# Optimization experiments

Measured on AMD Instinct MI355X. Metric: run time of the kernel, lower is better.

## Reference

```python
import jax, jax.numpy as jnp
import numpy as np


def setup_inputs() -> dict:
    key = jax.random.key(0)
    k1, k2 = jax.random.split(key)
    B, C, H, L = 4, 1, 1024, 4096
    x = jax.random.normal(k1, (B, H, L), dtype=jnp.float32)
    k = jax.random.normal(k2, (C, H, L), dtype=jnp.float32)
    return {"x": x, "k": k}


def reference(x, k):
    # x: (B, H, L) input; k: (C, H, l_kernel) SSM convolution kernel.
    # FFT convolution with zero-padding to n = l_kernel + L (linear conv),
    # then truncate to the first L outputs (causal conv output).
    L = x.shape[-1]
    l_kernel = k.shape[-1]
    n = l_kernel + L
    k_f = jnp.fft.rfft(k, n=n)                       # (C, H, n//2+1) complex
    x_f = jnp.fft.rfft(x, n=n)                       # (B, H, n//2+1) complex
    y_f = jnp.einsum('bhl,chl->bchl', x_f, k_f)      # broadcast complex multiply
    y = jnp.fft.irfft(y_f, n=n)[..., :L]             # (B, C, H, L)
    return y
```

## Files before the change

### kernel.cpp

```cpp
#include <hip/hip_runtime.h>

#define THREADS 256
#define B_DIM   4
#define H_DIM   1024
#define L_DIM   4096
#define NFFT    4096
#define PI_F     3.14159265358979323846f
#define TWO_PI_F 6.28318530717958647692f

__device__ __forceinline__ float2 cmulf(float2 a, float2 b) {
    return make_float2(a.x*b.x - a.y*b.y, a.x*b.y + a.y*b.x);
}
__device__ __forceinline__ float2 caddf(float2 a, float2 b){ return make_float2(a.x+b.x, a.y+b.y); }
__device__ __forceinline__ float2 csubf(float2 a, float2 b){ return make_float2(a.x-b.x, a.y-b.y); }

__device__ __forceinline__ int swz(int i) { return i ^ ((i>>4)&15) ^ ((i>>8)&15); }

__device__ __forceinline__ void make_tw(float base, float2 w[16]) {
    float sn, cs; __sincosf(base, &sn, &cs);
    w[1]  = make_float2(cs, sn);
    w[2]  = cmulf(w[1], w[1]);
    w[3]  = cmulf(w[2], w[1]);
    w[4]  = cmulf(w[2], w[2]);
    w[5]  = cmulf(w[4], w[1]);
    w[6]  = cmulf(w[4], w[2]);
    w[7]  = cmulf(w[4], w[3]);
    w[8]  = cmulf(w[4], w[4]);
    w[9]  = cmulf(w[8], w[1]);
    w[10] = cmulf(w[8], w[2]);
    w[11] = cmulf(w[8], w[3]);
    w[12] = cmulf(w[8], w[4]);
    w[13] = cmulf(w[8], w[5]);
    w[14] = cmulf(w[8], w[6]);
    w[15] = cmulf(w[8], w[7]);
}

__device__ __forceinline__ float2 w16c(int q, float s) {
    constexpr float C[8] = {1.f, 0.9238795325f, 0.7071067812f, 0.3826834324f,
                            0.f, -0.3826834324f, -0.7071067812f, -0.9238795325f};
    constexpr float S[8] = {0.f, 0.3826834324f, 0.7071067812f, 0.9238795325f,
                            1.f, 0.9238795325f, 0.7071067812f, 0.3826834324f};
    return make_float2(C[q], s*S[q]);
}

template<int SGN>
__device__ __forceinline__ float2 twq(float2 d, int q) {
    if (q == 0) return d;
    if (q == 4) return make_float2((float)(-SGN)*d.y, (float)SGN*d.x);
    return cmulf(d, w16c(q, (float)SGN));
}

template<int SGN, bool HZ>
__device__ __forceinline__ void dif16(float2 v[16]) {
    if (HZ) {
        #pragma unroll
        for (int i = 0; i < 8; ++i) {
            float2 a = v[i];
            v[i+8] = twq<SGN>(a, i);
        }
    } else {
        #pragma unroll
        for (int i = 0; i < 8; ++i) {
            float2 a = v[i], b = v[i+8];
            v[i]   = caddf(a,b);
            v[i+8] = twq<SGN>(csubf(a,b), i);
        }
    }
    #pragma unroll
    for (int h = 4; h >= 1; h >>= 1) {
        const int step = 8 / h;
        #pragma unroll
        for (int g = 0; g < 16; g += 2*h) {
            #pragma unroll
            for (int i = 0; i < h; ++i) {
                float2 a = v[g+i], b = v[g+i+h];
                v[g+i]   = caddf(a,b);
                v[g+i+h] = twq<SGN>(csubf(a,b), i*step);
            }
        }
    }
}

template<int SGN>
__device__ __forceinline__ void dit16(float2 v[16]) {
    #pragma unroll
    for (int h = 1; h <= 8; h <<= 1) {
        const int step = 8 / h;
        #pragma unroll
        for (int g = 0; g < 16; g += 2*h) {
            #pragma unroll
            for (int i = 0; i < h; ++i) {
                float2 a = v[g+i];
                float2 b = twq<SGN>(v[g+i+h], i*step);
                v[g+i]   = caddf(a,b);
                v[g+i+h] = csubf(a,b);
            }
        }
    }
}

__device__ __constant__ int REV4_C[16] = {0,8,4,12,2,10,6,14,1,9,5,13,3,11,7,15};

__device__ __forceinline__ void fwd_fft_row(const float2* __restrict__ src, float2* Z, int t) {
    constexpr int REV4[16] = {0,8,4,12,2,10,6,14,1,9,5,13,3,11,7,15};
    float2 v[16], w[16];
    #pragma unroll
    for (int r = 0; r < 8; ++r) v[r] = src[256*r + t];
    dif16<-1, true>(v);
    make_tw(-TWO_PI_F * (float)t / (float)NFFT, w);
    #pragma unroll
    for (int kk = 1; kk < 16; ++kk) v[REV4[kk]] = cmulf(v[REV4[kk]], w[kk]);
    #pragma unroll
    for (int kk = 0; kk < 16; ++kk) Z[swz(256*kk + t)] = v[REV4[kk]];
    __syncthreads();

    const int k1 = t >> 4, m = t & 15;
    const int rb = 256*k1 + m;
    #pragma unroll
    for (int r = 0; r < 16; ++r) v[r] = Z[swz(rb + 16*r)];
    dif16<-1,false>(v);
    make_tw(-TWO_PI_F * (float)m / 256.f, w);
    #pragma unroll
    for (int kk = 1; kk < 16; ++kk) v[REV4[kk]] = cmulf(v[REV4[kk]], w[kk]);
    #pragma unroll
    for (int kk = 0; kk < 16; ++kk) Z[swz(rb + 16*kk)] = v[REV4[kk]];
    __syncthreads();

    const int b3 = t << 4;
    #pragma unroll
    for (int r = 0; r < 16; ++r) v[r] = Z[swz(b3 + r)];
    dif16<-1,false>(v);
    #pragma unroll
    for (int kk = 0; kk < 16; ++kk) Z[swz(b3 + kk)] = v[REV4[kk]];
}

__device__ __forceinline__ int binpos(int j) {
    return swz( ((j&15)<<8) | (((j>>4)&15)<<4) | (j>>8) );
}

__global__ __launch_bounds__(THREADS, 4)
void kfft_kernel(const float* __restrict__ k, float2* __restrict__ Kf_all) {
    __shared__ float2 Zk[NFFT];
    const int t  = threadIdx.x;
    const int hh = blockIdx.x;
    const float2* kp = (const float2*)(k + (size_t)hh * L_DIM);

    fwd_fft_row(kp, Zk, t);
    __syncthreads();

    float2* Kf = Kf_all + (size_t)hh * NFFT;
    #pragma unroll
    for (int s = 0; s < 8; ++s) {
        int j = t + 256*s;
        if (j == 0) {
            float2 zk = Zk[0];
            Kf[0] = make_float2(zk.x + zk.y, zk.x - zk.y);
            float2 zk2 = Zk[swz(8)];
            Kf[2048] = make_float2(zk2.x, -zk2.y);
        } else {
            int jm = NFFT - j;
            float2 zkj = Zk[binpos(j)], zkm = Zk[binpos(jm)];
            float sn, cs; __sincosf(-PI_F * (float)j / (float)NFFT, &sn, &cs);
            float2 w = make_float2(cs, sn);
            float2 Ke = make_float2(0.5f*(zkj.x + zkm.x), 0.5f*(zkj.y - zkm.y));
            float2 dk = make_float2(zkj.x - zkm.x, zkj.y + zkm.y);
            float2 Ko = make_float2(0.5f*dk.y, -0.5f*dk.x);
            float2 tk = cmulf(w, Ko);
            Kf[j]  = caddf(Ke, tk);
            Kf[jm] = make_float2(Ke.x - tk.x, -(Ke.y - tk.y));
        }
    }
}

__global__ __launch_bounds__(THREADS, 4)
void conv_main_kernel(const float* __restrict__ x, const float2* __restrict__ Kf_all,
                      float* __restrict__ out) {
    __shared__ float2 Zx[NFFT];
    constexpr int REV4[16] = {0,8,4,12,2,10,6,14,1,9,5,13,3,11,7,15};

    const int t  = threadIdx.x;
    const int wg = blockIdx.x;
    const int hh = wg & (H_DIM - 1);
    const int b  = wg >> 10;

    const float2* xp = (const float2*)(x + ((size_t)(b*H_DIM + hh)) * L_DIM);
    const float2* Kf = Kf_all + (size_t)hh * NFFT;

    fwd_fft_row(xp, Zx, t);

    float2 kfj[8], kfm[8], kf2;
    #pragma unroll
    for (int s = 0; s < 8; ++s) {
        int j = t + 256*s;
        kfj[s] = Kf[j];
        kfm[s] = Kf[(NFFT - j) & (NFFT - 1)];
    }
    kf2 = Kf[2048];
    __syncthreads();

    #pragma unroll
    for (int s = 0; s < 8; ++s) {
        int j = t + 256*s;
        if (j == 0) {
            float2 zx = Zx[0];
            float ax0 = zx.x + zx.y, axM = zx.x - zx.y;
            float y0 = ax0 * kfj[0].x, yM = axM * kfj[0].y;
            Zx[0] = make_float2(0.5f*(y0 + yM), 0.5f*(y0 - yM));
            int p2 = swz(8);
            float2 zx2 = Zx[p2];
            Zx[p2] = cmulf(zx2, make_float2(kf2.x, -kf2.y));
        } else {
            int jm = NFFT - j;
            int pj = binpos(j), pm = binpos(jm);
            float2 zxj = Zx[pj], zxm = Zx[pm];

            float sn, cs; __sincosf(-PI_F * (float)j / (float)NFFT, &sn, &cs);
            float2 w = make_float2(cs, sn);

            float2 Xe = make_float2(0.5f*(zxj.x + zxm.x), 0.5f*(zxj.y - zxm.y));
            float2 dx = make_float2(zxj.x - zxm.x, zxj.y + zxm.y);
            float2 Xo = make_float2(0.5f*dx.y, -0.5f*dx.x);
            float2 tx = cmulf(w, Xo);
            float2 Axj = caddf(Xe, tx);
            float2 Axm = make_float2(Xe.x - tx.x, -(Xe.y - tx.y));

            float2 Yj = cmulf(Axj, kfj[s]);
            float2 Ym = cmulf(Axm, kfm[s]);

            float2 u  = make_float2(0.5f*(Yj.x + Ym.x), 0.5f*(Yj.y - Ym.y));
            float2 dd = make_float2(Yj.x - Ym.x, Yj.y + Ym.y);
            float2 wc = make_float2(w.x, -w.y);
            float2 vv = cmulf(wc, dd);
            vv.x *= 0.5f; vv.y *= 0.5f;
            Zx[pj] = make_float2(u.x - vv.y, u.y + vv.x);
            Zx[pm] = make_float2(u.x + vv.y, -(u.y - vv.x));
        }
    }
    __syncthreads();

    float2 vx[16], w[16];
    const int k1 = t >> 4, m = t & 15;
    const int rb = 256*k1 + m;
    const int b3 = t << 4;

    #pragma unroll
    for (int r = 0; r < 16; ++r) vx[REV4[r]] = Zx[swz(b3 + r)];
    dit16<1>(vx);
    #pragma unroll
    for (int mm = 0; mm < 16; ++mm) Zx[swz(b3 + mm)] = vx[mm];
    __syncthreads();

    make_tw(TWO_PI_F * (float)m / 256.f, w);
    #pragma unroll
    for (int kk = 0; kk < 16; ++kk) {
        float2 val = Zx[swz(rb + 16*kk)];
        if (kk > 0) val = cmulf(val, w[kk]);
        vx[REV4[kk]] = val;
    }
    dit16<1>(vx);
    #pragma unroll
    for (int r = 0; r < 16; ++r) Zx[swz(rb + 16*r)] = vx[r];
    __syncthreads();

    make_tw(TWO_PI_F * (float)t / (float)NFFT, w);
    #pragma unroll
    for (int kk = 0; kk < 16; ++kk) {
        float2 val = Zx[swz(256*kk + t)];
        if (kk > 0) val = cmulf(val, w[kk]);
        vx[REV4[kk]] = val;
    }
    dit16<1>(vx);
    float2* op = (float2*)(out + ((size_t)(b*H_DIM + hh)) * L_DIM);
    const float sc = 1.f / (float)NFFT;
    #pragma unroll
    for (int n1 = 0; n1 < 8; ++n1) {
        float2 z = vx[n1];
        op[256*n1 + t] = make_float2(z.x*sc, z.y*sc);
    }
}

__global__ __launch_bounds__(THREADS, 2)
void fftconv_fallback(const float* __restrict__ x, const float* __restrict__ k,
                      float* __restrict__ out) {
    __shared__ float2 Zx[NFFT];
    __shared__ float2 Zk[NFFT];
    constexpr int REV4[16] = {0,8,4,12,2,10,6,14,1,9,5,13,3,11,7,15};

    const int t  = threadIdx.x;
    const int wg = blockIdx.x;
    const int hh = wg & (H_DIM - 1);
    const int b  = wg >> 10;

    const float2* xp = (const float2*)(x + ((size_t)(b*H_DIM + hh)) * L_DIM);
    const float2* kp = (const float2*)(k + (size_t)hh * L_DIM);

    fwd_fft_row(xp, Zx, t);
    __syncthreads();
    fwd_fft_row(kp, Zk, t);
    __syncthreads();

    #pragma unroll
    for (int s = 0; s < 8; ++s) {
        int j = t + 256*s;
        if (j == 0) {
            float2 zx = Zx[0], zk = Zk[0];
            float ax0 = zx.x + zx.y, axM = zx.x - zx.y;
            float ak0 = zk.x + zk.y, akM = zk.x - zk.y;
            float y0 = ax0*ak0, yM = axM*akM;
            Zx[0] = make_float2(0.5f*(y0+yM), 0.5f*(y0-yM));
            int p2 = swz(8);
            Zx[p2] = cmulf(Zx[p2], Zk[p2]);
        } else {
            int jm = NFFT - j;
            int pj = binpos(j), pm = binpos(jm);
            float2 zxj = Zx[pj], zxm = Zx[pm];
            float2 zkj = Zk[pj], zkm = Zk[pm];
            float sn, cs; __sincosf(-PI_F * (float)j / (float)NFFT, &sn, &cs);
            float2 w = make_float2(cs, sn);
            float2 Xe = make_float2(0.5f*(zxj.x + zxm.x), 0.5f*(zxj.y - zxm.y));
            float2 dx = make_float2(zxj.x - zxm.x, zxj.y + zxm.y);
            float2 Xo = make_float2(0.5f*dx.y, -0.5f*dx.x);
            float2 tx = cmulf(w, Xo);
            float2 Axj = caddf(Xe, tx);
            float2 Axm = make_float2(Xe.x - tx.x, -(Xe.y - tx.y));
            float2 Ke = make_float2(0.5f*(zkj.x + zkm.x), 0.5f*(zkj.y - zkm.y));
            float2 dk = make_float2(zkj.x - zkm.x, zkj.y + zkm.y);
            float2 Ko = make_float2(0.5f*dk.y, -0.5f*dk.x);
            float2 tk = cmulf(w, Ko);
            float2 Akj = caddf(Ke, tk);
            float2 Akm = make_float2(Ke.x - tk.x, -(Ke.y - tk.y));
            float2 Yj = cmulf(Axj, Akj);
            float2 Ym = cmulf(Axm, Akm);
            float2 u  = make_float2(0.5f*(Yj.x + Ym.x), 0.5f*(Yj.y - Ym.y));
            float2 dd = make_float2(Yj.x - Ym.x, Yj.y + Ym.y);
            float2 wc = make_float2(w.x, -w.y);
            float2 vv = cmulf(wc, dd);
            vv.x *= 0.5f; vv.y *= 0.5f;
            Zx[pj] = make_float2(u.x - vv.y, u.y + vv.x);
            Zx[pm] = make_float2(u.x + vv.y, -(u.y - vv.x));
        }
    }
    __syncthreads();

    float2 vx[16], w[16];
    const int k1 = t >> 4, m = t & 15;
    const int rb = 256*k1 + m;
    const int b3 = t << 4;

    #pragma unroll
    for (int r = 0; r < 16; ++r) vx[REV4[r]] = Zx[swz(b3 + r)];
    dit16<1>(vx);
    #pragma unroll
    for (int mm = 0; mm < 16; ++mm) Zx[swz(b3 + mm)] = vx[mm];
    __syncthreads();

    make_tw(TWO_PI_F * (float)m / 256.f, w);
    #pragma unroll
    for (int kk = 0; kk < 16; ++kk) {
        float2 val = Zx[swz(rb + 16*kk)];
        if (kk > 0) val = cmulf(val, w[kk]);
        vx[REV4[kk]] = val;
    }
    dit16<1>(vx);
    #pragma unroll
    for (int r = 0; r < 16; ++r) Zx[swz(rb + 16*r)] = vx[r];
    __syncthreads();

    make_tw(TWO_PI_F * (float)t / (float)NFFT, w);
    #pragma unroll
    for (int kk = 0; kk < 16; ++kk) {
        float2 val = Zx[swz(256*kk + t)];
        if (kk > 0) val = cmulf(val, w[kk]);
        vx[REV4[kk]] = val;
    }
    dit16<1>(vx);
    float2* op = (float2*)(out + ((size_t)(b*H_DIM + hh)) * L_DIM);
    const float sc = 1.f / (float)NFFT;
    #pragma unroll
    for (int n1 = 0; n1 < 8; ++n1) {
        float2 z = vx[n1];
        op[256*n1 + t] = make_float2(z.x*sc, z.y*sc);
    }
}

extern "C" void kernel_launch(void* const* d_in, const int* in_sizes, int n_in,
                              void* d_out, int out_size, void* d_ws, size_t ws_size,
                              hipStream_t stream) {
    const float* x = (const float*)d_in[0];
    const float* k = (const float*)d_in[1];
    float* out = (float*)d_out;
    const size_t need = (size_t)H_DIM * NFFT * sizeof(float2);
    if (ws_size >= need) {
        float2* Kf = (float2*)d_ws;
        kfft_kernel<<<dim3(H_DIM), dim3(THREADS), 0, stream>>>(k, Kf);
        conv_main_kernel<<<dim3(B_DIM * H_DIM), dim3(THREADS), 0, stream>>>(x, Kf, out);
    } else {
        fftconv_fallback<<<dim3(B_DIM * H_DIM), dim3(THREADS), 0, stream>>>(x, k, out);
    }
}
```

Measured before the change: 176.3 us.

## Precompute P/Q kernel coefficients to fold real-FFT split into pointwise multiply

Replaces the Kf kernel-spectrum workspace with per-bin P/Q coefficients that combine the real-to-complex split/merge twiddles with the kernel spectrum and the 1/N scale. The main conv kernel then multiplies the packed complex FFT of x directly by P and Q using mirrored bins, so it skips separate post-processing and pre-inverse passes. It also drops the final scaling and keeps the kernel coefficients in registers loaded early, which overlaps the loads with the FFT stage. The cost is that the workspace doubles (float4 per bin), so more global data is read per block.

```diff
diff --git a/kernel.cpp b/kernel.cpp
--- a/kernel.cpp
+++ b/kernel.cpp
@@ -15,6 +15,10 @@
 __device__ __forceinline__ float2 csubf(float2 a, float2 b){ return make_float2(a.x-b.x, a.y-b.y); }
 
 __device__ __forceinline__ int swz(int i) { return i ^ ((i>>4)&15) ^ ((i>>8)&15); }
+
+__device__ __forceinline__ int drev12(int x) {
+    return ((x & 15) << 8) | (x & 0xF0) | (x >> 8);
+}
 
 __device__ __forceinline__ void make_tw(float base, float2 w[16]) {
     float sn, cs; __sincosf(base, &sn, &cs);
@@ -99,9 +103,7 @@
     }
 }
 
-__device__ __constant__ int REV4_C[16] = {0,8,4,12,2,10,6,14,1,9,5,13,3,11,7,15};
-
-__device__ __forceinline__ void fwd_fft_row(const float2* __restrict__ src, float2* Z, int t) {
+__device__ __forceinline__ void fwd_fft_12(const float2* __restrict__ src, float2* Z, int t) {
     constexpr int REV4[16] = {0,8,4,12,2,10,6,14,1,9,5,13,3,11,7,15};
     float2 v[16], w[16];
     #pragma unroll
@@ -125,7 +127,12 @@
     #pragma unroll
     for (int kk = 0; kk < 16; ++kk) Z[swz(rb + 16*kk)] = v[REV4[kk]];
     __syncthreads();
-
+}
+
+__device__ __forceinline__ void fwd_fft_row(const float2* __restrict__ src, float2* Z, int t) {
+    constexpr int REV4[16] = {0,8,4,12,2,10,6,14,1,9,5,13,3,11,7,15};
+    fwd_fft_12(src, Z, t);
+    float2 v[16];
     const int b3 = t << 4;
     #pragma unroll
     for (int r = 0; r < 16; ++r) v[r] = Z[swz(b3 + r)];
@@ -136,6 +143,136 @@
 
 __device__ __forceinline__ int binpos(int j) {
     return swz( ((j&15)<<8) | (((j>>4)&15)<<4) | (j>>8) );
+}
+
+
+__global__ __launch_bounds__(THREADS, 4)
+void kpq_kernel(const float* __restrict__ k, float4* __restrict__ PQ_all) {
+    __shared__ float2 Zk[NFFT];
+    constexpr int REV4[16] = {0,8,4,12,2,10,6,14,1,9,5,13,3,11,7,15};
+    const int t  = threadIdx.x;
+    const int hh = blockIdx.x;
+    const float2* kp = (const float2*)(k + (size_t)hh * L_DIM);
+
+    fwd_fft_12(kp, Zk, t);
+
+    const int b3 = t << 4;
+    float2 v[16];
+    #pragma unroll
+    for (int r = 0; r < 16; ++r) v[r] = Zk[swz(b3 + r)];
+    dif16<-1,false>(v);
+    #pragma unroll
+    for (int kk = 0; kk < 16; ++kk) Zk[swz(b3 + kk)] = v[REV4[kk]];
+    __syncthreads();
+
+    const int j1 = t & 15, j0 = t >> 4;
+    const int rdig = (j1 << 4) | j0;
+    const int C = t ? drev12(NFFT - rdig) : 16;
+    const int M = t ? (NFFT - 1) : 15;
+
+    float4* PQp = PQ_all + (size_t)hh * NFFT + b3;
+    const float sc = 1.f / (float)NFFT;
+
+    #pragma unroll
+    for (int kk = 0; kk < 16; ++kk) {
+        float2 Zj = v[REV4[kk]];
+        float2 zm = Zk[swz((C - kk) & M)];
+        float2 Zmc = make_float2(zm.x, -zm.y);
+
+        int j = (kk << 8) | rdig;
+        float sn, cs; __sincosf(-PI_F * (float)j / (float)NFFT, &sn, &cs);
+        const float c = cs, d = sn;
+        float2 u1 = make_float2(1.f + d, -c);
+        float2 u2 = make_float2(1.f - d,  c);
+        float2 A   = caddf(cmulf(u1, Zj), cmulf(u2, Zmc));
+        float2 Amc = caddf(cmulf(u2, Zj), cmulf(u1, Zmc));
+        float2 P = make_float2(0.25f*((1.f+d)*A.x + (1.f-d)*Amc.x),
+                               0.25f*((1.f+d)*A.y + (1.f-d)*Amc.y));
+        float2 dK = csubf(A, Amc);
+        float2 Q = make_float2(-0.25f*c*dK.y, 0.25f*c*dK.x);
+        PQp[kk] = make_float4(P.x*sc, P.y*sc, Q.x*sc, Q.y*sc);
+    }
+}
+
+__global__ __launch_bounds__(THREADS, 4)
+void conv_pq_kernel(const float* __restrict__ x, const float4* __restrict__ PQ_all,
+                    float* __restrict__ out) {
+    __shared__ float2 Zx[NFFT];
+    constexpr int REV4[16] = {0,8,4,12,2,10,6,14,1,9,5,13,3,11,7,15};
+
+    const int t  = threadIdx.x;
+    const int wg = blockIdx.x;
+    const int hh = wg & (H_DIM - 1);
+    const int b  = wg >> 10;
+
+    const float2* xp = (const float2*)(x + ((size_t)(b*H_DIM + hh)) * L_DIM);
+
+    fwd_fft_12(xp, Zx, t);
+
+    const float4* PQp = PQ_all + (size_t)hh * NFFT + (t << 4);
+    float4 pq[16];
+    #pragma unroll
+    for (int kk = 0; kk < 16; ++kk) pq[kk] = PQp[kk];
+
+    const int b3 = t << 4;
+    float2 v[16];
+    #pragma unroll
+    for (int r = 0; r < 16; ++r) v[r] = Zx[swz(b3 + r)];
+    dif16<-1,false>(v);
+    #pragma unroll
+    for (int kk = 0; kk < 16; ++kk) Zx[swz(b3 + kk)] = v[REV4[kk]];
+    __syncthreads();
+
+    const int j1 = t & 15, j0 = t >> 4;
+    const int rdig = (j1 << 4) | j0;
+    const int C = t ? drev12(NFFT - rdig) : 16;
+    const int M = t ? (NFFT - 1) : 15;
+
+    float2 vy[16];
+    #pragma unroll
+    for (int kk = 0; kk < 16; ++kk) {
+        float2 Zj = v[REV4[kk]];
+        float2 zm = Zx[swz((C - kk) & M)];
+        float2 P = make_float2(pq[kk].x, pq[kk].y);
+        float2 Q = make_float2(pq[kk].z, pq[kk].w);
+        float2 r1 = cmulf(P, Zj);
+        float2 r2 = make_float2(Q.x*zm.x + Q.y*zm.y, Q.y*zm.x - Q.x*zm.y);
+        vy[REV4[kk]] = caddf(r1, r2);
+    }
+    dit16<1>(vy);
+    __syncthreads();
+    #pragma unroll
+    for (int mm = 0; mm < 16; ++mm) Zx[swz(b3 + mm)] = vy[mm];
+    __syncthreads();
+
+    float2 vx[16], w[16];
+    const int k1 = t >> 4, m = t & 15;
+    const int rb = 256*k1 + m;
+    make_tw(TWO_PI_F * (float)m / 256.f, w);
+    #pragma unroll
+    for (int kk = 0; kk < 16; ++kk) {
+        float2 val = Zx[swz(rb + 16*kk)];
+        if (kk > 0) val = cmulf(val, w[kk]);
+        vx[REV4[kk]] = val;
+    }
+    dit16<1>(vx);
+    #pragma unroll
+    for (int r = 0; r < 16; ++r) Zx[swz(rb + 16*r)] = vx[r];
+    __syncthreads();
+
+    make_tw(TWO_PI_F * (float)t / (float)NFFT, w);
+    #pragma unroll
+    for (int kk = 0; kk < 16; ++kk) {
+        float2 val = Zx[swz(256*kk + t)];
+        if (kk > 0) val = cmulf(val, w[kk]);
+        vx[REV4[kk]] = val;
+    }
+    dit16<1>(vx);
+    float2* op = (float2*)(out + ((size_t)(b*H_DIM + hh)) * L_DIM);
+    #pragma unroll
+    for (int n1 = 0; n1 < 8; ++n1) {
+        op[256*n1 + t] = vx[n1];
+    }
 }
 
 __global__ __launch_bounds__(THREADS, 4)
@@ -389,8 +526,13 @@
     const float* x = (const float*)d_in[0];
     const float* k = (const float*)d_in[1];
     float* out = (float*)d_out;
-    const size_t need = (size_t)H_DIM * NFFT * sizeof(float2);
-    if (ws_size >= need) {
+    const size_t needPQ = (size_t)H_DIM * NFFT * sizeof(float4);
+    const size_t needKf = (size_t)H_DIM * NFFT * sizeof(float2);
+    if (ws_size >= needPQ) {
+        float4* PQ = (float4*)d_ws;
+        kpq_kernel<<<dim3(H_DIM), dim3(THREADS), 0, stream>>>(k, PQ);
+        conv_pq_kernel<<<dim3(B_DIM * H_DIM), dim3(THREADS), 0, stream>>>(x, PQ, out);
+    } else if (ws_size >= needKf) {
         float2* Kf = (float2*)d_ws;
         kfft_kernel<<<dim3(H_DIM), dim3(THREADS), 0, stream>>>(k, Kf);
         conv_main_kernel<<<dim3(B_DIM * H_DIM), dim3(THREADS), 0, stream>>>(x, Kf, out);
```

Result: slower. 279.9 us (+58.8%).
